# Kernel tuning notes

Measured on AMD Instinct MI355X. Metric: run time of the kernel, lower is better.

Reference implementation:

```python
import math
import jax, jax.numpy as jnp
import numpy as np

B, H, SQ, SK, D, M = 2, 16, 2048, 2048, 128, 128

def setup_inputs() -> dict:
    key = jax.random.key(0)
    kq, kk, ks = jax.random.split(key, 3)
    q = jax.random.normal(kq, (B, H, SQ, D), dtype=jnp.float32)
    k = jax.random.normal(kk, (B, H, SK, D), dtype=jnp.float32)
    # Gaussian projection matrix S of shape (m, dim), as in generate_projection_matrix
    S = jax.random.normal(ks, (M, D), dtype=jnp.float32)
    return {"q": q, "k": k, "S": S}


def reference(q, k, S):
    """QJL: quantize keys to sign bits + norm, then asymmetric inner-product estimate.

    quantize(k):  sign_bits = sign(k @ S.T) with sign(0) -> +1;  norm_k = ||k||_2
    estimate:     <q,k> ~= <S q, sign(S k)> * (sqrt(pi/2)/m) * ||k||
    """
    m = S.shape[0]
    scale = np.float32(math.sqrt(math.pi / 2.0)) / np.float32(m)
    # --- quantize keys ---
    norm_k = jnp.linalg.norm(k, axis=-1)                      # (B,H,SK)
    proj_k = jnp.einsum('bhkd,md->bhkm', k, S)                # (B,H,SK,M)
    sign_bits = jnp.where(proj_k >= 0, 1.0, -1.0).astype(jnp.float32)
    # --- project queries (asymmetric, no quantization) ---
    Sq = jnp.einsum('bhqd,md->bhqm', q, S)                    # (B,H,SQ,M)
    # --- estimate inner products: (Sq * signs).sum(-1) for every (q, k) pair ---
    dots = jnp.einsum('bhqm,bhkm->bhqk', Sq, sign_bits)       # (B,H,SQ,SK)
    estimated = dots * scale * norm_k[:, :, None, :]
    return estimated
```

## Files before the change

kernel.cpp:

```cpp
#include <hip/hip_runtime.h>
#include <hip/hip_bf16.h>
#include <math.h>

#define NBH   32
#define SEQ   2048
#define DD    128
#define MM    128

typedef unsigned short u16;
typedef unsigned int   u32;
typedef float  f32x4  __attribute__((ext_vector_type(4)));
typedef __bf16 bf16x8 __attribute__((ext_vector_type(8)));

#define SCALE_F 0.009791516697777346f
#define TAU 0.18f
#define CCAP 2048

static __device__ __forceinline__ u16 f2bf(float f) {
  union { float f; u32 u; } v; v.f = f;
  u32 u = v.u;
  u += 0x7fffu + ((u >> 16) & 1u);
  return (u16)(u >> 16);
}

static __device__ __forceinline__ u16 f64_sign(const float* __restrict__ K,
                                               const float* __restrict__ S,
                                               int row_g, int m) {
  const f32x4* kr = (const f32x4*)(K + (size_t)row_g * DD);
  const f32x4* sr = (const f32x4*)(S + (size_t)m * DD);
  double a0 = 0, a1 = 0, a2 = 0, a3 = 0;
#pragma unroll
  for (int d = 0; d < 32; d += 4) {
    f32x4 x0 = kr[d],   y0 = sr[d];
    f32x4 x1 = kr[d+1], y1 = sr[d+1];
    f32x4 x2 = kr[d+2], y2 = sr[d+2];
    f32x4 x3 = kr[d+3], y3 = sr[d+3];
    a0 += (double)x0.x*y0.x + (double)x0.y*y0.y + (double)x0.z*y0.z + (double)x0.w*y0.w;
    a1 += (double)x1.x*y1.x + (double)x1.y*y1.y + (double)x1.z*y1.z + (double)x1.w*y1.w;
    a2 += (double)x2.x*y2.x + (double)x2.y*y2.y + (double)x2.z*y2.z + (double)x2.w*y2.w;
    a3 += (double)x3.x*y3.x + (double)x3.y*y3.y + (double)x3.z*y3.z + (double)x3.w*y3.w;
  }
  return (((a0 + a1) + (a2 + a3)) >= 0.0) ? 0x3F80 : 0xBF80;
}

static __device__ __forceinline__ void mfma_tile(const u16* lA, const u16* lB,
                                                 int wave, int lane,
                                                 f32x4 acc[4][4]) {
  const int wr = wave >> 1, wc = wave & 1;
  const int lrow = lane & 15, lkg = lane >> 4;
#pragma unroll
  for (int kk = 0; kk < 4; ++kk) {
    bf16x8 af[4], bfr[4];
    const int c = kk * 4 + lkg;
#pragma unroll
    for (int a = 0; a < 4; ++a) {
      const int r  = wr * 64 + a * 16 + lrow;
      const int r2 = wc * 64 + a * 16 + lrow;
      af[a]  = *(const bf16x8*)((const char*)lA + r  * 256 + ((c ^ (r  & 7)) << 4));
      bfr[a] = *(const bf16x8*)((const char*)lB + r2 * 256 + ((c ^ (r2 & 7)) << 4));
    }
#pragma unroll
    for (int a = 0; a < 4; ++a)
#pragma unroll
      for (int b = 0; b < 4; ++b)
        acc[a][b] = __builtin_amdgcn_mfma_f32_16x16x32_bf16(af[a], bfr[b], acc[a][b], 0, 0, 0);
  }
}

static __device__ __forceinline__ void stage_f32_to_bf16(const float* __restrict__ src,
                                                         u16* lds, int tid) {
#pragma unroll
  for (int j = 0; j < 8; ++j) {
    int i = tid + j * 256;
    int r = i >> 4, c = i & 15;
    const f32x4* gp = (const f32x4*)(src + (size_t)r * DD + c * 8);
    f32x4 v0 = gp[0], v1 = gp[1];
    union { u16 h[8]; f32x4 v; } pk;
    pk.h[0] = f2bf(v0.x); pk.h[1] = f2bf(v0.y); pk.h[2] = f2bf(v0.z); pk.h[3] = f2bf(v0.w);
    pk.h[4] = f2bf(v1.x); pk.h[5] = f2bf(v1.y); pk.h[6] = f2bf(v1.z); pk.h[7] = f2bf(v1.w);
    *(f32x4*)((char*)lds + r * 256 + ((c ^ (r & 7)) << 4)) = pk.v;
  }
}

__global__ __launch_bounds__(256) void k_proj(
    const float* __restrict__ Q, const float* __restrict__ K,
    const float* __restrict__ S, u16* __restrict__ Sqb, u16* __restrict__ Sgn,
    float* __restrict__ sn) {
  __shared__ __align__(16) u16 lds2[2 * 128 * 128];
  __shared__ u16 cbuf[CCAP];
  __shared__ u32 lcnt;
  u16* lA = lds2;
  u16* lB = lds2 + 128 * 128;
  const int tid = threadIdx.x;
  const int tile = blockIdx.x;
  const bool isK = (tile >= 512);
  const int row0 = (isK ? (tile - 512) : tile) * 128;
  const float* src = isK ? K : Q;

  if (tid == 0) lcnt = 0;

  stage_f32_to_bf16(S, lB, tid);
  stage_f32_to_bf16(src + (size_t)row0 * DD, lA, tid);

  if (isK) {
    const int row = tid >> 1, half = tid & 1;
    const f32x4* base = (const f32x4*)(src + (size_t)(row0 + row) * DD) + half * 16;
    float s = 0.f;
#pragma unroll
    for (int j = 0; j < 16; ++j) {
      f32x4 v = base[j];
      s += v.x * v.x + v.y * v.y + v.z * v.z + v.w * v.w;
    }
    s += __shfl_xor(s, 1);
    if (half == 0) sn[row0 + row] = SCALE_F * sqrtf(s);
  }
  __syncthreads();

  const int wave = tid >> 6, lane = tid & 63;
  f32x4 acc[4][4];
#pragma unroll
  for (int a = 0; a < 4; ++a)
#pragma unroll
    for (int b = 0; b < 4; ++b) acc[a][b] = (f32x4){0.f, 0.f, 0.f, 0.f};

  mfma_tile(lA, lB, wave, lane, acc);

  __syncthreads();
  float* lc = (float*)lds2;
  const int wr = wave >> 1, wc = wave & 1;
#pragma unroll
  for (int a = 0; a < 4; ++a) {
#pragma unroll
    for (int b = 0; b < 4; ++b) {
      const int col = wc * 64 + b * 16 + (lane & 15);
#pragma unroll
      for (int j = 0; j < 4; ++j) {
        const int row = wr * 64 + a * 16 + (lane >> 4) * 4 + j;
        lc[row * 128 + (col ^ (((row >> 2) & 1) << 4))] = acc[a][b][j];
      }
    }
  }
  __syncthreads();

  const int c8 = tid & 15;
  const int rr = tid >> 4;
#pragma unroll
  for (int p = 0; p < 8; ++p) {
    const int row = rr + p * 16;
    const int s = (row >> 2) & 1;
    const int cb = (c8 ^ (s << 1)) * 8;
    f32x4 v0 = *(const f32x4*)&lc[row * 128 + cb];
    f32x4 v1 = *(const f32x4*)&lc[row * 128 + cb + 4];
    float vals[8] = {v0.x, v0.y, v0.z, v0.w, v1.x, v1.y, v1.z, v1.w};
    union { u16 h[8]; f32x4 v; } pk;
    const int row_g = row0 + row;
    if (!isK) {
#pragma unroll
      for (int e = 0; e < 8; ++e) pk.h[e] = f2bf(vals[e]);
      *(f32x4*)(Sqb + (size_t)row_g * MM + c8 * 8) = pk.v;
    } else {
#pragma unroll
      for (int e = 0; e < 8; ++e) {
        const int m = c8 * 8 + e;
        u16 sg = (vals[e] >= 0.f) ? 0x3F80 : 0xBF80;
        if (fabsf(vals[e]) < TAU) {
          u32 pos = atomicAdd(&lcnt, 1u);
          if (pos < CCAP) cbuf[pos] = (u16)((row << 7) | m);
          else sg = f64_sign(K, S, row_g, m);
        }
        pk.h[e] = sg;
      }
      *(f32x4*)(Sgn + (size_t)row_g * MM + c8 * 8) = pk.v;
    }
  }

  if (isK) {
    __syncthreads();
    u32 n = lcnt; if (n > CCAP) n = CCAP;
    for (u32 i = tid; i < n; i += 256) {
      u32 code = cbuf[i];
      int r = code >> 7, m = code & 127;
      Sgn[(size_t)(row0 + r) * MM + m] = f64_sign(K, S, row0 + r, m);
    }
  }
}

__global__ __launch_bounds__(256) void k_gemm(
    const u16* __restrict__ Sqb, const u16* __restrict__ Sgn,
    const float* __restrict__ sn, float* __restrict__ out) {
  __shared__ __align__(16) u16 lds2[2 * 128 * 128];
  u16* lA = lds2;
  u16* lB = lds2 + 128 * 128;
  const int tid = threadIdx.x;
  const u32 id = blockIdx.x;
  const u32 l = (id & 7) * 1024 + (id >> 3);
  const int tn = l & 15, tm = (l >> 4) & 15, bh = l >> 8;
  const u16* Abase = Sqb + ((size_t)bh * SEQ + tm * 128) * MM;
  const u16* Bbase = Sgn + ((size_t)bh * SEQ + tn * 128) * MM;

  {
    typedef __attribute__((address_space(3))) char lds_t;
    typedef const __attribute__((address_space(1))) char glob_t;
    const int wv = tid >> 6, ln = tid & 63;
#pragma unroll
    for (int j = 0; j < 8; ++j) {
      const int s = j * 256 + wv * 64 + ln;
      const int r = s >> 4, cp = s & 15;
      const int srcoff = r * 256 + ((cp ^ (r & 7)) << 4);
      __builtin_amdgcn_global_load_lds((glob_t*)((const char*)Abase + srcoff),
                                       (lds_t*)((char*)lA + s * 16), 16, 0, 0);
      __builtin_amdgcn_global_load_lds((glob_t*)((const char*)Bbase + srcoff),
                                       (lds_t*)((char*)lB + s * 16), 16, 0, 0);
    }
  }
  __syncthreads();

  const int wave = tid >> 6, lane = tid & 63;
  f32x4 acc[4][4];
#pragma unroll
  for (int a = 0; a < 4; ++a)
#pragma unroll
    for (int b = 0; b < 4; ++b) acc[a][b] = (f32x4){0.f, 0.f, 0.f, 0.f};

  mfma_tile(lA, lB, wave, lane, acc);

  __syncthreads();
  float* lc = (float*)lds2;
  const int wr = wave >> 1, wc = wave & 1;
#pragma unroll
  for (int a = 0; a < 4; ++a) {
#pragma unroll
    for (int b = 0; b < 4; ++b) {
      const int col = wc * 64 + b * 16 + (lane & 15);
#pragma unroll
      for (int j = 0; j < 4; ++j) {
        const int row = wr * 64 + a * 16 + (lane >> 4) * 4 + j;
        lc[row * 128 + (col ^ (((row >> 2) & 1) << 4))] = acc[a][b][j];
      }
    }
  }
  __syncthreads();

  const float* snb = sn + bh * SEQ + tn * 128;
  const size_t outbase = (size_t)bh * SEQ * SEQ + (size_t)tm * 128 * SEQ + tn * 128;
  const int c = tid & 31;
  const int r0 = tid >> 5;
  const f32x4 s4 = *(const f32x4*)(snb + c * 4);
#pragma unroll
  for (int p = 0; p < 16; ++p) {
    const int row = r0 + p * 8;
    const int cs = c ^ (((row >> 2) & 1) << 2);
    f32x4 v = *(const f32x4*)&lc[row * 128 + cs * 4];
    v = v * s4;
    __builtin_nontemporal_store(v, (f32x4*)(out + outbase + (size_t)row * SEQ + c * 4));
  }
}

extern "C" void kernel_launch(void* const* d_in, const int* in_sizes, int n_in,
                              void* d_out, int out_size, void* d_ws, size_t ws_size,
                              hipStream_t stream) {
  const float* q = (const float*)d_in[0];
  const float* k = (const float*)d_in[1];
  const float* S = (const float*)d_in[2];
  float* out = (float*)d_out;
  char* ws = (char*)d_ws;

  const size_t off_Sq  = 0;
  const size_t off_Sg  = 16777216;
  const size_t off_sn  = 33554432;

  u16*   Sqb = (u16*)(ws + off_Sq);
  u16*   Sgn = (u16*)(ws + off_Sg);
  float* sn  = (float*)(ws + off_sn);

  k_proj<<<1024, 256, 0, stream>>>(q, k, S, Sqb, Sgn, sn);
  k_gemm<<<8192, 256, 0, stream>>>(Sqb, Sgn, sn, out);
}
```

Before: 157.7 us.

## Pack key signs into bits and shrink GEMM LDS footprint for occupancy

Key sign matrix is stored as one bit per entry instead of bf16, and the GEMM kernel expands the bits to ±1 bf16 in registers while loading B fragments. The f64 fallback now flips provisional bits with atomicXor. The epilogue writes the accumulator tile in two halves through a 32 KB buffer, so LDS per block drops to about 34 KB and launch bounds ask for 4 blocks per CU. This cuts sign-matrix traffic and LDS pressure, at the cost of extra ALU work to unpack the bits and an extra barrier round in the epilogue.

```diff
diff --git a/kernel.cpp b/kernel.cpp
--- a/kernel.cpp
+++ b/kernel.cpp
@@ -9,6 +9,7 @@
 
 typedef unsigned short u16;
 typedef unsigned int   u32;
+typedef unsigned char  u8;
 typedef float  f32x4  __attribute__((ext_vector_type(4)));
 typedef __bf16 bf16x8 __attribute__((ext_vector_type(8)));
 
@@ -23,9 +24,9 @@
   return (u16)(u >> 16);
 }
 
-static __device__ __forceinline__ u16 f64_sign(const float* __restrict__ K,
-                                               const float* __restrict__ S,
-                                               int row_g, int m) {
+static __device__ __forceinline__ u32 f64_negbit(const float* __restrict__ K,
+                                                 const float* __restrict__ S,
+                                                 int row_g, int m) {
   const f32x4* kr = (const f32x4*)(K + (size_t)row_g * DD);
   const f32x4* sr = (const f32x4*)(S + (size_t)m * DD);
   double a0 = 0, a1 = 0, a2 = 0, a3 = 0;
@@ -40,7 +41,7 @@
     a2 += (double)x2.x*y2.x + (double)x2.y*y2.y + (double)x2.z*y2.z + (double)x2.w*y2.w;
     a3 += (double)x3.x*y3.x + (double)x3.y*y3.y + (double)x3.z*y3.z + (double)x3.w*y3.w;
   }
-  return (((a0 + a1) + (a2 + a3)) >= 0.0) ? 0x3F80 : 0xBF80;
+  return (((a0 + a1) + (a2 + a3)) < 0.0) ? 1u : 0u;
 }
 
 static __device__ __forceinline__ void mfma_tile(const u16* lA, const u16* lB,
@@ -84,7 +85,7 @@
 
 __global__ __launch_bounds__(256) void k_proj(
     const float* __restrict__ Q, const float* __restrict__ K,
-    const float* __restrict__ S, u16* __restrict__ Sqb, u16* __restrict__ Sgn,
+    const float* __restrict__ S, u16* __restrict__ Sqb, u8* __restrict__ Sgb,
     float* __restrict__ sn) {
   __shared__ __align__(16) u16 lds2[2 * 128 * 128];
   __shared__ u16 cbuf[CCAP];
@@ -152,51 +153,56 @@
     f32x4 v0 = *(const f32x4*)&lc[row * 128 + cb];
     f32x4 v1 = *(const f32x4*)&lc[row * 128 + cb + 4];
     float vals[8] = {v0.x, v0.y, v0.z, v0.w, v1.x, v1.y, v1.z, v1.w};
-    union { u16 h[8]; f32x4 v; } pk;
     const int row_g = row0 + row;
     if (!isK) {
+      union { u16 h[8]; f32x4 v; } pk;
 #pragma unroll
       for (int e = 0; e < 8; ++e) pk.h[e] = f2bf(vals[e]);
       *(f32x4*)(Sqb + (size_t)row_g * MM + c8 * 8) = pk.v;
     } else {
+      u32 byteval = 0;
 #pragma unroll
       for (int e = 0; e < 8; ++e) {
         const int m = c8 * 8 + e;
-        u16 sg = (vals[e] >= 0.f) ? 0x3F80 : 0xBF80;
+        u32 bitneg = (vals[e] < 0.f) ? 1u : 0u;
         if (fabsf(vals[e]) < TAU) {
           u32 pos = atomicAdd(&lcnt, 1u);
-          if (pos < CCAP) cbuf[pos] = (u16)((row << 7) | m);
-          else sg = f64_sign(K, S, row_g, m);
+          if (pos < CCAP) cbuf[pos] = (u16)((row << 8) | (bitneg << 7) | m);
+          else bitneg = f64_negbit(K, S, row_g, m);
         }
-        pk.h[e] = sg;
+        byteval |= bitneg << e;
       }
-      *(f32x4*)(Sgn + (size_t)row_g * MM + c8 * 8) = pk.v;
+      Sgb[(size_t)row_g * 16 + c8] = (u8)byteval;
     }
   }
 
   if (isK) {
     __syncthreads();
+    __threadfence();
     u32 n = lcnt; if (n > CCAP) n = CCAP;
+    u32* Sg32 = (u32*)Sgb;
     for (u32 i = tid; i < n; i += 256) {
       u32 code = cbuf[i];
-      int r = code >> 7, m = code & 127;
-      Sgn[(size_t)(row0 + r) * MM + m] = f64_sign(K, S, row0 + r, m);
-    }
-  }
-}
-
-__global__ __launch_bounds__(256) void k_gemm(
-    const u16* __restrict__ Sqb, const u16* __restrict__ Sgn,
+      int r = (code >> 8) & 127, m = code & 127;
+      u32 prov = (code >> 7) & 1;
+      u32 f64b = f64_negbit(K, S, row0 + r, m);
+      if (f64b != prov)
+        atomicXor(Sg32 + (size_t)(row0 + r) * 4 + (m >> 5), 1u << (m & 31));
+    }
+  }
+}
+
+__global__ __launch_bounds__(256, 4) void k_gemm(
+    const u16* __restrict__ Sqb, const u8* __restrict__ Sgb,
     const float* __restrict__ sn, float* __restrict__ out) {
-  __shared__ __align__(16) u16 lds2[2 * 128 * 128];
-  u16* lA = lds2;
-  u16* lB = lds2 + 128 * 128;
+  __shared__ __align__(16) char smem[32768 + 2048];
+  const u32* lBb = (const u32*)(smem + 32768);
   const int tid = threadIdx.x;
   const u32 id = blockIdx.x;
   const u32 l = (id & 7) * 1024 + (id >> 3);
   const int tn = l & 15, tm = (l >> 4) & 15, bh = l >> 8;
-  const u16* Abase = Sqb + ((size_t)bh * SEQ + tm * 128) * MM;
-  const u16* Bbase = Sgn + ((size_t)bh * SEQ + tn * 128) * MM;
+  const char* Abase = (const char*)(Sqb + ((size_t)bh * SEQ + tm * 128) * MM);
+  const char* Bbase = (const char*)(Sgb + ((size_t)bh * SEQ + tn * 128) * 16);
 
   {
     typedef __attribute__((address_space(3))) char lds_t;
@@ -207,52 +213,80 @@
       const int s = j * 256 + wv * 64 + ln;
       const int r = s >> 4, cp = s & 15;
       const int srcoff = r * 256 + ((cp ^ (r & 7)) << 4);
-      __builtin_amdgcn_global_load_lds((glob_t*)((const char*)Abase + srcoff),
-                                       (lds_t*)((char*)lA + s * 16), 16, 0, 0);
-      __builtin_amdgcn_global_load_lds((glob_t*)((const char*)Bbase + srcoff),
-                                       (lds_t*)((char*)lB + s * 16), 16, 0, 0);
-    }
+      __builtin_amdgcn_global_load_lds((glob_t*)(Abase + srcoff),
+                                       (lds_t*)(smem + s * 16), 16, 0, 0);
+    }
+    if (tid < 128)
+      __builtin_amdgcn_global_load_lds((glob_t*)(Bbase + tid * 16),
+                                       (lds_t*)(smem + 32768 + tid * 16), 16, 0, 0);
   }
   __syncthreads();
 
   const int wave = tid >> 6, lane = tid & 63;
+  const int wr = wave >> 1, wc = wave & 1;
+  const int lrow = lane & 15, lkg = lane >> 4;
   f32x4 acc[4][4];
 #pragma unroll
   for (int a = 0; a < 4; ++a)
 #pragma unroll
     for (int b = 0; b < 4; ++b) acc[a][b] = (f32x4){0.f, 0.f, 0.f, 0.f};
 
-  mfma_tile(lA, lB, wave, lane, acc);
-
-  __syncthreads();
-  float* lc = (float*)lds2;
-  const int wr = wave >> 1, wc = wave & 1;
-#pragma unroll
-  for (int a = 0; a < 4; ++a) {
-#pragma unroll
-    for (int b = 0; b < 4; ++b) {
-      const int col = wc * 64 + b * 16 + (lane & 15);
-#pragma unroll
-      for (int j = 0; j < 4; ++j) {
-        const int row = wr * 64 + a * 16 + (lane >> 4) * 4 + j;
-        lc[row * 128 + (col ^ (((row >> 2) & 1) << 4))] = acc[a][b][j];
-      }
-    }
-  }
-  __syncthreads();
+#pragma unroll
+  for (int kk = 0; kk < 4; ++kk) {
+    const int c = kk * 4 + lkg;
+    bf16x8 af[4], bfr[4];
+#pragma unroll
+    for (int a = 0; a < 4; ++a) {
+      const int r = wr * 64 + a * 16 + lrow;
+      af[a] = *(const bf16x8*)(smem + r * 256 + ((c ^ (r & 7)) << 4));
+      const int r2 = wc * 64 + a * 16 + lrow;
+      u32 word = lBb[r2 * 4 + kk];
+      u32 byte = (word >> (lkg * 8)) & 0xFFu;
+      union { u16 h[8]; bf16x8 v; } ub;
+#pragma unroll
+      for (int e = 0; e < 8; ++e) ub.h[e] = ((byte >> e) & 1u) ? 0xBF80 : 0x3F80;
+      bfr[a] = ub.v;
+    }
+#pragma unroll
+    for (int a = 0; a < 4; ++a)
+#pragma unroll
+      for (int b = 0; b < 4; ++b)
+        acc[a][b] = __builtin_amdgcn_mfma_f32_16x16x32_bf16(af[a], bfr[b], acc[a][b], 0, 0, 0);
+  }
 
   const float* snb = sn + bh * SEQ + tn * 128;
   const size_t outbase = (size_t)bh * SEQ * SEQ + (size_t)tm * 128 * SEQ + tn * 128;
-  const int c = tid & 31;
-  const int r0 = tid >> 5;
-  const f32x4 s4 = *(const f32x4*)(snb + c * 4);
-#pragma unroll
-  for (int p = 0; p < 16; ++p) {
-    const int row = r0 + p * 8;
-    const int cs = c ^ (((row >> 2) & 1) << 2);
-    f32x4 v = *(const f32x4*)&lc[row * 128 + cs * 4];
-    v = v * s4;
-    __builtin_nontemporal_store(v, (f32x4*)(out + outbase + (size_t)row * SEQ + c * 4));
+  const int cch = tid & 31;
+  const int hr0 = tid >> 5;
+  const f32x4 s4 = *(const f32x4*)(snb + cch * 4);
+  float* lc = (float*)smem;
+
+#pragma unroll
+  for (int h = 0; h < 2; ++h) {
+    __syncthreads();
+#pragma unroll
+    for (int a2 = 0; a2 < 2; ++a2) {
+      const int a = 2 * h + a2;
+#pragma unroll
+      for (int b = 0; b < 4; ++b) {
+        const int col = wc * 64 + b * 16 + (lane & 15);
+#pragma unroll
+        for (int j = 0; j < 4; ++j) {
+          const int hr = wr * 32 + a2 * 16 + (lane >> 4) * 4 + j;
+          lc[hr * 128 + (col ^ (((hr >> 2) & 1) << 4))] = acc[a][b][j];
+        }
+      }
+    }
+    __syncthreads();
+#pragma unroll
+    for (int p = 0; p < 8; ++p) {
+      const int hr = hr0 + p * 8;
+      const int row = ((hr >> 5) << 6) + 32 * h + (hr & 31);
+      const int cs = cch ^ (((hr >> 2) & 1) << 2);
+      f32x4 v = *(const f32x4*)&lc[hr * 128 + cs * 4];
+      v = v * s4;
+      __builtin_nontemporal_store(v, (f32x4*)(out + outbase + (size_t)row * SEQ + cch * 4));
+    }
   }
 }
 
@@ -267,12 +301,12 @@
 
   const size_t off_Sq  = 0;
   const size_t off_Sg  = 16777216;
-  const size_t off_sn  = 33554432;
+  const size_t off_sn  = 17825792;
 
   u16*   Sqb = (u16*)(ws + off_Sq);
-  u16*   Sgn = (u16*)(ws + off_Sg);
+  u8*    Sgb = (u8*)(ws + off_Sg);
   float* sn  = (float*)(ws + off_sn);
 
-  k_proj<<<1024, 256, 0, stream>>>(q, k, S, Sqb, Sgn, sn);
-  k_gemm<<<8192, 256, 0, stream>>>(Sqb, Sgn, sn, out);
-}
+  k_proj<<<1024, 256, 0, stream>>>(q, k, S, Sqb, Sgb, sn);
+  k_gemm<<<8192, 256, 0, stream>>>(Sqb, Sgb, sn, out);
+}
```

Result: slower. 163.0 us (+3.3%).
